# Optimization experiments

Hardware: AMD Instinct MI355X
Metric: run time of the kernel (lower is better)

Reference implementation:

```python
import jax, jax.numpy as jnp
import numpy as np

S, B, D, NH = 4096, 4, 1024, 16


def _unitnorm(v):
    # v / ||v||_2 along last dim (matches torch.norm(v, dim=-1))
    return v / jnp.linalg.norm(v, axis=-1, keepdims=True)


def setup_inputs() -> dict:
    key = jax.random.key(0)
    ks = jax.random.split(key, 9)
    scale = 1.0 / np.sqrt(D)
    inp = {
        "h": jax.random.normal(ks[0], (S, B, D), dtype=jnp.float32),
        "Wq_w": jax.random.normal(ks[1], (D, D), dtype=jnp.float32) * scale,
        "Wq_b": jax.random.normal(ks[2], (D,), dtype=jnp.float32) * scale,
        "Wk_w": jax.random.normal(ks[3], (D, D), dtype=jnp.float32) * scale,
        "Wk_b": jax.random.normal(ks[4], (D,), dtype=jnp.float32) * scale,
        "Wv_w": jax.random.normal(ks[5], (D, D), dtype=jnp.float32) * scale,
        "Wv_b": jax.random.normal(ks[6], (D,), dtype=jnp.float32) * scale,
        "Wo_w": jax.random.normal(ks[7], (D, D), dtype=jnp.float32) * scale,
        "Wo_b": jax.random.normal(ks[8], (D,), dtype=jnp.float32) * scale,
        "nhead": NH,
    }
    return inp


def reference(h, Wq_w, Wq_b, Wk_w, Wk_b, Wv_w, Wv_b, Wo_w, Wo_b, nhead):
    s, b, d = h.shape
    dh = d // nhead

    def proj(W, bias):
        # torch nn.Linear: x @ W.T + b, then split heads -> [S,B,NH,dh]
        return (h @ W.T + bias).reshape(s, b, nhead, dh)

    k = jax.nn.elu(_unitnorm(proj(Wk_w, Wk_b)))  # unitelu
    v = proj(Wv_w, Wv_b)
    q = _unitnorm(proj(Wq_w, Wq_b))  # sigma = unitnorm (default)

    # Linear-attention state: sum of outer products over the whole sequence
    A = jnp.einsum('sbnq,sbnv->bnvq', k, v)  # [B,NH,dh,dh]
    out = jnp.einsum('sbnq,bnvq->sbnv', q, A).reshape(s, b, d)
    out = out @ Wo_w.T + Wo_b
    return out, k, q
```

## Files before the change

kernel.cpp:

```cpp
#include <hip/hip_runtime.h>
#include <hip/hip_bf16.h>
#include <math.h>

#define S_LEN 4096
#define B_SZ  4
#define D_DIM 1024
#define NHEAD 16
#define R_ROWS (S_LEN * B_SZ)

#define AS1 __attribute__((address_space(1)))
#define AS3 __attribute__((address_space(3)))

typedef __bf16 bf16_t;
typedef __attribute__((ext_vector_type(8))) __bf16 bf16x8;
typedef __attribute__((ext_vector_type(4))) __bf16 bf16x4;
typedef __attribute__((ext_vector_type(4))) float  f32x4;

#define MFMA16 __builtin_amdgcn_mfma_f32_16x16x32_bf16

__device__ __forceinline__ void gload16(const bf16_t* g, bf16_t* l) {
  __builtin_amdgcn_global_load_lds((const AS1 unsigned int*)g,
                                   (AS3 unsigned int*)l, 16, 0, 0);
}

#define BAR asm volatile("s_barrier" ::: "memory")
#define LGKM0 do { asm volatile("s_waitcnt lgkmcnt(0)" ::: "memory"); \
                   __builtin_amdgcn_sched_barrier(0); } while (0)

#define RD_A(dst, ap, mlo) \
  _Pragma("unroll") for (int mm = 0; mm < 4; ++mm) \
    _Pragma("unroll") for (int kx = 0; kx < 2; ++kx) \
      dst[mm][kx] = *(const bf16x8*)&ap[offA[(mlo) + mm][kx]];
#define RD_B(dst, bp, nlo) \
  _Pragma("unroll") for (int nn = 0; nn < 2; ++nn) \
    _Pragma("unroll") for (int kx = 0; kx < 2; ++kx) \
      dst[nn][kx] = *(const bf16x8*)&bp[offB[(nlo) + nn][kx]];
#define QUAD(mb, nb, AF, BF) \
  do { __builtin_amdgcn_s_setprio(1); \
  _Pragma("unroll") for (int mm = 0; mm < 4; ++mm) \
    _Pragma("unroll") for (int nn = 0; nn < 2; ++nn) { \
      acc[(mb)+mm][(nb)+nn] = MFMA16(AF[mm][0], BF[nn][0], acc[(mb)+mm][(nb)+nn], 0, 0, 0); \
      acc[(mb)+mm][(nb)+nn] = MFMA16(AF[mm][1], BF[nn][1], acc[(mb)+mm][(nb)+nn], 0, 0, 0); } \
  __builtin_amdgcn_s_setprio(0); } while (0)

__global__ void k_cvt(const float* __restrict__ src, bf16_t* __restrict__ dst, int n) {
  int i = (blockIdx.x * 256 + threadIdx.x) * 4;
  if (i >= n) return;
  f32x4 v = *(const f32x4*)(src + i);
  bf16x4 o;
  o[0] = (bf16_t)v[0]; o[1] = (bf16_t)v[1]; o[2] = (bf16_t)v[2]; o[3] = (bf16_t)v[3];
  *(bf16x4*)(dst + i) = o;
}

__device__ __forceinline__ void gemm_core_8ph(
    const bf16_t* __restrict__ A, const bf16_t* __restrict__ B,
    int row0, int col0,
    bf16_t (&sA)[2][2][8192], bf16_t (&sB)[2][2][8192], f32x4 (&acc)[8][4])
{
  const int tid  = threadIdx.x;
  const int wave = tid >> 6, lane = tid & 63;
  const int lr = lane & 15, lg = lane >> 4;
  const int wr = wave >> 2, wn = wave & 3;
  const int grow = tid >> 3;
  const int gsw  = (tid & 7) ^ (grow & 7);

  auto stA = [&](int buf, int half, int k0) {
    #pragma unroll
    for (int j = 0; j < 2; ++j)
      gload16(&A[(size_t)(row0 + half * 128 + j * 64 + grow) * D_DIM + k0 + gsw * 8],
              &sA[buf][half][(j * 64 + wave * 8) * 64]);
  };
  auto stB = [&](int buf, int half, int k0) {
    #pragma unroll
    for (int j = 0; j < 2; ++j)
      gload16(&B[(size_t)(col0 + half * 128 + j * 64 + grow) * D_DIM + k0 + gsw * 8],
              &sB[buf][half][(j * 64 + wave * 8) * 64]);
  };

  int offA[8][2], offB[4][2];
  #pragma unroll
  for (int m = 0; m < 8; ++m) {
    const int r = m * 16 + lr;
    #pragma unroll
    for (int kx = 0; kx < 2; ++kx)
      offA[m][kx] = r * 64 + (((kx << 2) + lg) ^ (r & 7)) * 8;
  }
  #pragma unroll
  for (int n = 0; n < 4; ++n) {
    const int r = (wn & 1) * 64 + n * 16 + lr;
    #pragma unroll
    for (int kx = 0; kx < 2; ++kx)
      offB[n][kx] = r * 64 + (((kx << 2) + lg) ^ (r & 7)) * 8;
  }
  const bf16_t* a0 = &sA[0][wr][0];
  const bf16_t* a1 = &sA[1][wr][0];
  const bf16_t* b0 = &sB[0][wn >> 1][0];
  const bf16_t* b1 = &sB[1][wn >> 1][0];

  #pragma unroll
  for (int m = 0; m < 8; m++)
    #pragma unroll
    for (int n = 0; n < 4; n++)
      #pragma unroll
      for (int r = 0; r < 4; r++) acc[m][n][r] = 0.f;

  stA(0, 0, 0);  stA(0, 1, 0);  stB(0, 0, 0);  stB(0, 1, 0);
  stA(1, 0, 64); stA(1, 1, 64); stB(1, 0, 64); stB(1, 1, 64);
  asm volatile("s_waitcnt vmcnt(8)" ::: "memory");
  BAR;

  bf16x8 af03[4][2], af47[4][2], bf01[2][2], bf23[2][2];

  #pragma unroll 1
  for (int i = 0; i < 8; ++i) {
    const bool last = (i == 7);
    const int kn0 = (i + 1) * 128, kn1 = kn0 + 64;

    RD_A(af03, a0, 0); RD_B(bf01, b0, 0);
    BAR; LGKM0; QUAD(0, 0, af03, bf01); BAR;
    RD_A(af47, a0, 4);
    BAR; LGKM0; QUAD(4, 0, af47, bf01); BAR;
    RD_B(bf23, b0, 2);
    if (!last) stA(0, 0, kn0);
    BAR; LGKM0; QUAD(0, 2, af03, bf23); BAR;
    if (!last) { stA(0, 1, kn0); stB(0, 0, kn0); }
    BAR; QUAD(4, 2, af47, bf23);
    if (!last) asm volatile("s_waitcnt vmcnt(6)" ::: "memory");
    else       asm volatile("s_waitcnt vmcnt(0)" ::: "memory");
    BAR;

    RD_A(af03, a1, 0); RD_B(bf01, b1, 0);
    if (!last) stB(0, 1, kn0);
    BAR; LGKM0; QUAD(0, 0, af03, bf01); BAR;
    RD_A(af47, a1, 4);
    BAR; LGKM0; QUAD(4, 0, af47, bf01); BAR;
    RD_B(bf23, b1, 2);
    if (!last) stA(1, 0, kn1);
    BAR; LGKM0; QUAD(0, 2, af03, bf23); BAR;
    if (!last) { stA(1, 1, kn1); stB(1, 0, kn1); stB(1, 1, kn1); }
    BAR; QUAD(4, 2, af47, bf23);
    if (!last) asm volatile("s_waitcnt vmcnt(8)" ::: "memory");
    BAR;
  }
}

__global__ __launch_bounds__(512, 2) void k_proj(
    const bf16_t* __restrict__ hB, const bf16_t* __restrict__ Wcat,
    const float* __restrict__ bq, const float* __restrict__ bk, const float* __restrict__ bv,
    bf16_t* __restrict__ outVb, float* __restrict__ outK, float* __restrict__ outQ,
    bf16_t* __restrict__ qBm)
{
  __shared__ bf16_t sA[2][2][8192];
  __shared__ bf16_t sB[2][2][8192];

  const int tid  = threadIdx.x;
  const int wave = tid >> 6, lane = tid & 63;
  const int lr = lane & 15, lg = lane >> 4;
  const int wr = wave >> 2, wn = wave & 3;
  const int row0 = blockIdx.x * 256;
  const int by   = blockIdx.y;

  f32x4 acc[8][4];
  gemm_core_8ph(hB, Wcat, row0, by * 256, sA, sB, acc);

  const int sec = by >> 2;
  const int hc0 = (by & 3) * 256 + wn * 64;
  const float* bias = (sec == 0) ? bq : (sec == 1 ? bk : bv);
  float bvv[4];
  #pragma unroll
  for (int n = 0; n < 4; n++) bvv[n] = bias[hc0 + n * 16 + lr];

  #pragma unroll
  for (int m = 0; m < 8; ++m) {
    #pragma unroll
    for (int r = 0; r < 4; ++r) {
      const int gm = row0 + wr * 128 + m * 16 + lg * 4 + r;
      float v[4];
      float ss = 0.f;
      #pragma unroll
      for (int n = 0; n < 4; n++) {
        v[n] = acc[m][n][r] + bvv[n];
        ss += v[n] * v[n];
      }
      if (sec == 2) {
        #pragma unroll
        for (int n = 0; n < 4; n++)
          outVb[(size_t)gm * D_DIM + hc0 + n * 16 + lr] = (bf16_t)v[n];
      } else {
        #pragma unroll
        for (int msk = 1; msk < 16; msk <<= 1) ss += __shfl_xor(ss, msk);
        const float rs = 1.0f / sqrtf(ss);
        if (sec == 0) {
          const size_t qrow = (size_t)(gm & 3) * S_LEN + (gm >> 2);
          #pragma unroll
          for (int n = 0; n < 4; n++) {
            const float qn = v[n] * rs;
            outQ[(size_t)gm * D_DIM + hc0 + n * 16 + lr] = qn;
            qBm[qrow * D_DIM + hc0 + n * 16 + lr] = (bf16_t)qn;
          }
        } else {
          #pragma unroll
          for (int n = 0; n < 4; n++) {
            float kn = v[n] * rs;
            kn = kn > 0.f ? kn : expm1f(kn);
            outK[(size_t)gm * D_DIM + hc0 + n * 16 + lr] = kn;
          }
        }
      }
    }
  }
}

__global__ __launch_bounds__(256) void k_state(
    const float* __restrict__ Kf, const bf16_t* __restrict__ Vb,
    float* __restrict__ Apart)
{
  const int bn = blockIdx.x;
  const int ch = blockIdx.y;
  const int b = bn >> 4, n = bn & 15;
  const int tid = threadIdx.x;
  const int ti = tid >> 4, tj = tid & 15;

  __shared__ float sV[32][64];
  __shared__ float sK[32][64];

  float acc[4][4];
  #pragma unroll
  for (int i = 0; i < 4; i++)
    #pragma unroll
    for (int j = 0; j < 4; j++) acc[i][j] = 0.f;

  const int rr = tid >> 3, cc = (tid & 7) * 8;
  for (int s0 = ch * 512; s0 < ch * 512 + 512; s0 += 32) {
    const size_t g = (size_t)((s0 + rr) * B_SZ + b) * D_DIM + n * 64 + cc;
    bf16x8 v8 = *(const bf16x8*)&Vb[g];
    #pragma unroll
    for (int e = 0; e < 8; e++) sV[rr][cc + e] = (float)v8[e];
    *(f32x4*)&sK[rr][cc]     = *(const f32x4*)&Kf[g];
    *(f32x4*)&sK[rr][cc + 4] = *(const f32x4*)&Kf[g + 4];
    __syncthreads();
    #pragma unroll
    for (int ss = 0; ss < 32; ss++) {
      f32x4 vv = *(const f32x4*)&sV[ss][ti * 4];
      f32x4 kk = *(const f32x4*)&sK[ss][tj * 4];
      #pragma unroll
      for (int i = 0; i < 4; i++)
        #pragma unroll
        for (int j = 0; j < 4; j++)
          acc[i][j] = fmaf(vv[i], kk[j], acc[i][j]);
    }
    __syncthreads();
  }
  float* ap = Apart + ((size_t)ch * 64 + bn) * 4096;
  #pragma unroll
  for (int i = 0; i < 4; i++)
    #pragma unroll
    for (int j = 0; j < 4; j++)
      ap[(ti * 4 + i) * 64 + tj * 4 + j] = acc[i][j];
}

__global__ __launch_bounds__(256) void k_combine(
    const float* __restrict__ Apart, const bf16_t* __restrict__ WoB,
    bf16_t* __restrict__ Ct)
{
  const int bn = blockIdx.x;
  const int dp = blockIdx.y;
  const int b = bn >> 4, n = bn & 15;
  const int tid = threadIdx.x;
  const int ti = tid >> 4, tj = tid & 15;

  __shared__ float sAm[64][65];
  __shared__ float sW[64][65];

  #pragma unroll
  for (int p = 0; p < 16; p++) {
    const int idx = tid + p * 256;
    float s = 0.f;
    #pragma unroll
    for (int c2 = 0; c2 < 8; c2++)
      s += Apart[((size_t)c2 * 64 + bn) * 4096 + idx];
    sAm[idx >> 6][idx & 63] = s;
  }
  {
    const int r = tid >> 2, cv = (tid & 3) * 16;
    bf16x8 w0 = *(const bf16x8*)&WoB[(size_t)(dp * 64 + r) * D_DIM + n * 64 + cv];
    bf16x8 w1 = *(const bf16x8*)&WoB[(size_t)(dp * 64 + r) * D_DIM + n * 64 + cv + 8];
    #pragma unroll
    for (int e = 0; e < 8; e++) {
      sW[r][cv + e]     = (float)w0[e];
      sW[r][cv + 8 + e] = (float)w1[e];
    }
  }
  __syncthreads();

  float acc[4][4];
  #pragma unroll
  for (int i = 0; i < 4; i++)
    #pragma unroll
    for (int j = 0; j < 4; j++) acc[i][j] = 0.f;

  for (int dv = 0; dv < 64; dv++) {
    float w[4], a[4];
    #pragma unroll
    for (int i = 0; i < 4; i++) w[i] = sW[ti * 4 + i][dv];
    #pragma unroll
    for (int j = 0; j < 4; j++) a[j] = sAm[dv][tj * 4 + j];
    #pragma unroll
    for (int i = 0; i < 4; i++)
      #pragma unroll
      for (int j = 0; j < 4; j++)
        acc[i][j] = fmaf(w[i], a[j], acc[i][j]);
  }
  #pragma unroll
  for (int i = 0; i < 4; i++)
    #pragma unroll
    for (int j = 0; j < 4; j++)
      Ct[((size_t)b * D_DIM + dp * 64 + ti * 4 + i) * D_DIM + n * 64 + tj * 4 + j] =
          (bf16_t)acc[i][j];
}

__global__ __launch_bounds__(512, 2) void k_final(
    const bf16_t* __restrict__ qBm, const bf16_t* __restrict__ Ct,
    const float* __restrict__ bo, float* __restrict__ outO)
{
  __shared__ bf16_t sA[2][2][8192];
  __shared__ bf16_t sB[2][2][8192];

  const int tid  = threadIdx.x;
  const int wave = tid >> 6, lane = tid & 63;
  const int lr = lane & 15, lg = lane >> 4;
  const int wr = wave >> 2, wn = wave & 3;
  const int b    = blockIdx.z;
  const int row0 = blockIdx.x * 256;
  const int col0 = blockIdx.y * 256;

  f32x4 acc[8][4];
  gemm_core_8ph(qBm + (size_t)b * S_LEN * D_DIM, Ct + (size_t)b * D_DIM * D_DIM,
                row0, col0, sA, sB, acc);

  #pragma unroll
  for (int m = 0; m < 8; ++m) {
    #pragma unroll
    for (int r = 0; r < 4; ++r) {
      const int gs = row0 + wr * 128 + m * 16 + lg * 4 + r;
      #pragma unroll
      for (int n = 0; n < 4; n++) {
        const int col = col0 + wn * 64 + n * 16 + lr;
        outO[((size_t)gs * B_SZ + b) * D_DIM + col] = acc[m][n][r] + bo[col];
      }
    }
  }
}

extern "C" void kernel_launch(void* const* d_in, const int* in_sizes, int n_in,
                              void* d_out, int out_size, void* d_ws, size_t ws_size,
                              hipStream_t stream) {
  (void)in_sizes; (void)n_in; (void)out_size; (void)ws_size;
  const float* h  = (const float*)d_in[0];
  const float* Wq = (const float*)d_in[1];
  const float* bq = (const float*)d_in[2];
  const float* Wk = (const float*)d_in[3];
  const float* bk = (const float*)d_in[4];
  const float* Wv = (const float*)d_in[5];
  const float* bv = (const float*)d_in[6];
  const float* Wo = (const float*)d_in[7];
  const float* bo = (const float*)d_in[8];

  float* out0 = (float*)d_out;
  float* outK = out0 + (size_t)R_ROWS * D_DIM;
  float* outQ = outK + (size_t)R_ROWS * D_DIM;
  bf16_t* vB  = (bf16_t*)d_out;

  char* ws = (char*)d_ws;
  bf16_t* hB    = (bf16_t*)ws;
  bf16_t* Ct    = (bf16_t*)ws;
  bf16_t* Wcat  = (bf16_t*)(ws + 33554432);
  bf16_t* WoB   = (bf16_t*)(ws + 33554432 + 6291456);
  float*  Apart = (float*)(ws + 41943040);
  bf16_t* qBm   = (bf16_t*)(ws + 50331648);

  const int nH = R_ROWS * D_DIM;
  const int nW = D_DIM * D_DIM;
  k_cvt<<<nH / 1024, 256, 0, stream>>>(h, hB, nH);
  k_cvt<<<nW / 1024, 256, 0, stream>>>(Wq, Wcat, nW);
  k_cvt<<<nW / 1024, 256, 0, stream>>>(Wk, Wcat + nW, nW);
  k_cvt<<<nW / 1024, 256, 0, stream>>>(Wv, Wcat + 2 * nW, nW);
  k_cvt<<<nW / 1024, 256, 0, stream>>>(Wo, WoB, nW);

  k_proj<<<dim3(R_ROWS / 256, 12), 512, 0, stream>>>(hB, Wcat, bq, bk, bv,
                                                     vB, outK, outQ, qBm);
  k_state<<<dim3(64, 8), 256, 0, stream>>>(outK, vB, Apart);
  k_combine<<<dim3(64, 16), 256, 0, stream>>>(Apart, WoB, Ct);
  k_final<<<dim3(S_LEN / 256, D_DIM / 256, B_SZ), 512, 0, stream>>>(qBm, Ct, bo, out0);
}
```

Measured before the change: 254.4 us.

## Remap projection blocks across XCDs and use inline-asm LDS reads

Adds an XCD-aware block index remap in the projection GEMM so that blocks dispatched round-robin to the 8 chiplets handle contiguous tiles. Neighbouring tiles then share the A rows and weight columns in each chiplet's L2. It also replaces the LDS fragment loads with explicit ds_read_b128 inline asm on precomputed byte addresses, to cut address arithmetic and control instruction selection. The inline asm hides these loads from the compiler's dependency tracking, so correctness depends on the existing manual lgkmcnt waits. The grid shape stays 64x12 while the mapping changes.

```diff
diff --git a/kernel.cpp b/kernel.cpp
--- a/kernel.cpp
+++ b/kernel.cpp
@@ -22,19 +22,24 @@
   __builtin_amdgcn_global_load_lds((const AS1 unsigned int*)g,
                                    (AS3 unsigned int*)l, 16, 0, 0);
 }
+__device__ __forceinline__ bf16x8 ldsr(unsigned a) {
+  bf16x8 r;
+  asm volatile("ds_read_b128 %0, %1" : "=v"(r) : "v"(a));
+  return r;
+}
 
 #define BAR asm volatile("s_barrier" ::: "memory")
 #define LGKM0 do { asm volatile("s_waitcnt lgkmcnt(0)" ::: "memory"); \
                    __builtin_amdgcn_sched_barrier(0); } while (0)
 
-#define RD_A(dst, ap, mlo) \
+#define RD_A(dst, ab, mlo) \
   _Pragma("unroll") for (int mm = 0; mm < 4; ++mm) \
     _Pragma("unroll") for (int kx = 0; kx < 2; ++kx) \
-      dst[mm][kx] = *(const bf16x8*)&ap[offA[(mlo) + mm][kx]];
-#define RD_B(dst, bp, nlo) \
+      dst[mm][kx] = ldsr((ab) + offAb[(mlo) + mm][kx]);
+#define RD_B(dst, bb, nlo) \
   _Pragma("unroll") for (int nn = 0; nn < 2; ++nn) \
     _Pragma("unroll") for (int kx = 0; kx < 2; ++kx) \
-      dst[nn][kx] = *(const bf16x8*)&bp[offB[(nlo) + nn][kx]];
+      dst[nn][kx] = ldsr((bb) + offBb[(nlo) + nn][kx]);
 #define QUAD(mb, nb, AF, BF) \
   do { __builtin_amdgcn_s_setprio(1); \
   _Pragma("unroll") for (int mm = 0; mm < 4; ++mm) \
@@ -77,25 +82,27 @@
               &sB[buf][half][(j * 64 + wave * 8) * 64]);
   };
 
-  int offA[8][2], offB[4][2];
+  unsigned offAb[8][2], offBb[4][2];
   #pragma unroll
   for (int m = 0; m < 8; ++m) {
     const int r = m * 16 + lr;
     #pragma unroll
     for (int kx = 0; kx < 2; ++kx)
-      offA[m][kx] = r * 64 + (((kx << 2) + lg) ^ (r & 7)) * 8;
+      offAb[m][kx] = (unsigned)((r * 64 + (((kx << 2) + lg) ^ (r & 7)) * 8) * 2);
   }
   #pragma unroll
   for (int n = 0; n < 4; ++n) {
     const int r = (wn & 1) * 64 + n * 16 + lr;
     #pragma unroll
     for (int kx = 0; kx < 2; ++kx)
-      offB[n][kx] = r * 64 + (((kx << 2) + lg) ^ (r & 7)) * 8;
-  }
-  const bf16_t* a0 = &sA[0][wr][0];
-  const bf16_t* a1 = &sA[1][wr][0];
-  const bf16_t* b0 = &sB[0][wn >> 1][0];
-  const bf16_t* b1 = &sB[1][wn >> 1][0];
+      offBb[n][kx] = (unsigned)((r * 64 + (((kx << 2) + lg) ^ (r & 7)) * 8) * 2);
+  }
+  const unsigned baseA = (unsigned)(uintptr_t)&sA[0][0][0];
+  const unsigned baseB = (unsigned)(uintptr_t)&sB[0][0][0];
+  const unsigned a0 = baseA + (unsigned)wr * 16384u;
+  const unsigned a1 = baseA + 32768u + (unsigned)wr * 16384u;
+  const unsigned b0 = baseB + (unsigned)(wn >> 1) * 16384u;
+  const unsigned b1 = baseB + 32768u + (unsigned)(wn >> 1) * 16384u;
 
   #pragma unroll
   for (int m = 0; m < 8; m++)
@@ -157,8 +164,12 @@
   const int wave = tid >> 6, lane = tid & 63;
   const int lr = lane & 15, lg = lane >> 4;
   const int wr = wave >> 2, wn = wave & 3;
-  const int row0 = blockIdx.x * 256;
-  const int by   = blockIdx.y;
+
+  const int launched = blockIdx.x + blockIdx.y * gridDim.x;
+  const int L  = (launched & 7) * 96 + (launched >> 3);
+  const int by = L >> 6;
+  const int bx = L & 63;
+  const int row0 = bx * 256;
 
   f32x4 acc[8][4];
   gemm_core_8ph(hB, Wcat, row0, by * 256, sA, sB, acc);
@@ -387,8 +398,8 @@
   k_cvt<<<nW / 1024, 256, 0, stream>>>(Wv, Wcat + 2 * nW, nW);
   k_cvt<<<nW / 1024, 256, 0, stream>>>(Wo, WoB, nW);
 
-  k_proj<<<dim3(R_ROWS / 256, 12), 512, 0, stream>>>(hB, Wcat, bq, bk, bv,
-                                                     vB, outK, outQ, qBm);
+  k_proj<<<dim3(64, 12), 512, 0, stream>>>(hB, Wcat, bq, bk, bv,
+                                           vB, outK, outQ, qBm);
   k_state<<<dim3(64, 8), 256, 0, stream>>>(outK, vB, Apart);
   k_combine<<<dim3(64, 16), 256, 0, stream>>>(Apart, WoB, Ct);
   k_final<<<dim3(S_LEN / 256, D_DIM / 256, B_SZ), 512, 0, stream>>>(qBm, Ct, bo, out0);
```

After: 582.1 us. 2.29x slower.
